# Performance work log

Hardware: AMD Instinct MI355X
Metric: run time of the kernel (lower is better)

The kernel has to match this reference:

```python
import jax, jax.numpy as jnp
import numpy as np
import math

B, S, D, H = 4, 512, 1024, 16
DH = D // H
DQ = D // 4
MIN_STEPS, MAX_STEPS = 4, 12
THR = 1e-4


def lin(t, w, b):
    # torch Linear convention: w is (out, in)
    return jnp.einsum('...i,oi->...o', t, w) + b


def gelu(t):
    return jax.nn.gelu(t, approximate=False)  # torch nn.GELU() exact


def layernorm(t, g, b):
    m = t.mean(-1, keepdims=True)
    v = jnp.mean(jnp.square(t - m), axis=-1, keepdims=True)
    return (t - m) * jax.lax.rsqrt(v + 1e-5) * g + b


def _forward(h, x, ig_w1, ig_b1, ig_w2, ig_b2, wq, bq, wk, bk, wv, bv, wo, bo,
             g1_w1, g1_b1, g1_w2, g1_b2, gate_logits, ln_g, ln_b,
             sp_w1, sp_b1, sp_w2, sp_b2):
    # adaptive step count: steps = base + floor(sigmoid(MLP(mean_pool(h))).mean() * extra)
    pooled = h.mean(axis=1)  # (B, D)
    extra = jax.nn.sigmoid(lin(gelu(lin(pooled, sp_w1, sp_b1)), sp_w2, sp_b2)).mean()
    num_steps = jnp.minimum(
        MIN_STEPS + jnp.floor(extra * (MAX_STEPS - MIN_STEPS)).astype(jnp.int32), MAX_STEPS)

    gw = jax.nn.softmax(gate_logits)  # gate weights over the 3 gates
    scale = 1.0 / math.sqrt(DH)

    def step(carry, i):
        h, active = carry
        # G1 gate (G2/G3 multiply zero memory/expert outputs -> drop)
        G1 = jax.nn.sigmoid(lin(gelu(lin(h, g1_w1, g1_b1)), g1_w2, g1_b2)) * gw[0]
        # Phi: input-gated blend + raw multi-head self-attention
        gate = jax.nn.sigmoid(
            lin(gelu(lin(jnp.concatenate([h, x], axis=-1), ig_w1, ig_b1)), ig_w2, ig_b2))
        blended = gate * h + (1.0 - gate) * x
        q = lin(blended, wq, bq).reshape(B, S, H, DH)
        k = lin(blended, wk, bk).reshape(B, S, H, DH)
        v = lin(blended, wv, bv).reshape(B, S, H, DH)
        attn = jax.nn.softmax(jnp.einsum('bqhd,bkhd->bhqk', q, k) * scale, axis=-1)
        ctx = jnp.einsum('bhqk,bkhd->bqhd', attn, v).reshape(B, S, D)
        phi = lin(ctx, wo, bo)
        h_new = layernorm(h + G1 * phi, ln_g, ln_b)
        res = jnp.linalg.norm(h_new - h) / (jnp.linalg.norm(h) + 1e-8)
        act_i = active & (i < num_steps)
        h = jnp.where(act_i, h_new, h)
        active = act_i & jnp.logical_not((i >= MIN_STEPS) & (res < THR))
        return (h, active), None

    (h, _), _ = jax.lax.scan(step, (h, jnp.array(True)), jnp.arange(MAX_STEPS))
    return h


def setup_inputs() -> dict:
    key = jax.random.key(0)
    ks = jax.random.split(key, 16)
    f32 = jnp.float32

    def W(k, out_d, in_d):
        return jax.random.normal(k, (out_d, in_d), f32) * (1.0 / np.sqrt(in_d))

    return {
        'h': jax.random.normal(ks[0], (B, S, D), f32),
        'x': jax.random.normal(ks[1], (B, S, D), f32),
        # PhiLayer input_gate: Linear(2D, D/4) -> GELU -> Linear(D/4, D) -> Sigmoid
        'ig_w1': W(ks[2], DQ, 2 * D), 'ig_b1': jnp.zeros((DQ,), f32),
        'ig_w2': W(ks[3], D, DQ), 'ig_b2': jnp.zeros((D,), f32),
        # QKV / out projections (xavier-ish, zero bias)
        'wq': W(ks[4], D, D), 'bq': jnp.zeros((D,), f32),
        'wk': W(ks[5], D, D), 'bk': jnp.zeros((D,), f32),
        'wv': W(ks[6], D, D), 'bv': jnp.zeros((D,), f32),
        'wo': W(ks[7], D, D), 'bo': jnp.zeros((D,), f32),
        # Gating gate #1 MLP (only G1 contributes; memory/experts are zero)
        'g1_w1': W(ks[8], DQ, D), 'g1_b1': jnp.zeros((DQ,), f32),
        'g1_w2': W(ks[9], D, DQ), 'g1_b2': jnp.zeros((D,), f32),
        'gate_logits': jnp.ones((3,), f32),  # nn.Parameter(torch.ones(3))
        # LayerNorm
        'ln_g': jnp.ones((D,), f32), 'ln_b': jnp.zeros((D,), f32),
        # step predictor: Linear(D, D/4) -> GELU -> Linear(D/4, 1)
        'sp_w1': W(ks[10], DQ, D), 'sp_b1': jnp.zeros((DQ,), f32),
        'sp_w2': W(ks[11], 1, DQ), 'sp_b2': jnp.zeros((1,), f32),
    }


def reference(h, x, ig_w1, ig_b1, ig_w2, ig_b2, wq, bq, wk, bk, wv, bv, wo, bo,
              g1_w1, g1_b1, g1_w2, g1_b2, gate_logits, ln_g, ln_b,
              sp_w1, sp_b1, sp_w2, sp_b2):
    return _forward(h, x, ig_w1, ig_b1, ig_w2, ig_b2, wq, bq, wk, bk, wv, bv, wo, bo,
                    g1_w1, g1_b1, g1_w2, g1_b2, gate_logits, ln_g, ln_b,
                    sp_w1, sp_b1, sp_w2, sp_b2)
```

## Files before the change

kernel.cpp:

```cpp
#include <hip/hip_runtime.h>
#include <hip/hip_bf16.h>


#define B_   4
#define S_   512
#define D_   1024
#define H_   16
#define DH_  64
#define MSEQ 2048
#define GRID_ 512

typedef short short8 __attribute__((ext_vector_type(8)));
typedef float floatx4 __attribute__((ext_vector_type(4)));

static constexpr size_t OFF_H    = 0;
static constexpr size_t OFF_X    = 2097152;
static constexpr size_t OFF_HXB  = 4194304;
static constexpr size_t OFF_T2B  = 6291456;
static constexpr size_t OFF_T1B  = 6553600;
static constexpr size_t OFF_G1B  = 6815744;
static constexpr size_t OFF_QKVB = 7864320;
static constexpr size_t OFF_U    = 7864320;
static constexpr size_t OFF_CTXB = 11010048;
static constexpr size_t OFF_WARE = 12058624;
static constexpr size_t OFF_BIAS = 14811136;
static constexpr size_t OFF_POOL = 14817792;
static constexpr size_t OFF_SPT  = 14821888;
static constexpr size_t OFF_PPART= 14822912;
static constexpr size_t OFF_SCAL = 14888448;
static constexpr size_t OFF_XIG  = 14888960;

static constexpr int W_WIG1 = 0;
static constexpr int W_WIG2 = 524288;
static constexpr int W_WG1  = 786432;
static constexpr int W_WG2  = 1048576;
static constexpr int W_QKV  = 1310720;
static constexpr int W_WO   = 4456448;
static constexpr int W_TOT  = 5505024;
static constexpr int B_TOT  = 6656;

__device__ __forceinline__ float bf2f(unsigned int u) {
  return __uint_as_float((u & 0xFFFFu) << 16);
}
__device__ __forceinline__ short f2bs(float f) {
  __hip_bfloat16 b = __float2bfloat16(f);
  return *reinterpret_cast<short*>(&b);
}
__device__ __forceinline__ unsigned int pk2(float lo, float hi) {
  return (unsigned int)(unsigned short)f2bs(lo) | ((unsigned int)(unsigned short)f2bs(hi) << 16);
}
__device__ __forceinline__ float ldf(const void* p, size_t i, int f32m) {
  return f32m ? ((const float*)p)[i] : bf2f(((const unsigned short*)p)[i]);
}
__device__ __forceinline__ int f32mode(const void* lng) {
  return (((const unsigned int*)lng)[0] == 0x3F800000u) ? 1 : 0;
}
__device__ __forceinline__ float gelu_f(float x) {
  return 0.5f * x * (1.0f + erff(x * 0.70710678118654752440f));
}
__device__ __forceinline__ float sig_f(float x) {
  return 1.0f / (1.0f + expf(-x));
}
__device__ __forceinline__ void gl_lds16(const short* gp, short* lp) {
  __builtin_amdgcn_global_load_lds(
      (const __attribute__((address_space(1))) unsigned int*)gp,
      (__attribute__((address_space(3))) unsigned int*)lp, 16, 0, 0);
}
__device__ __forceinline__ float wave_sum(float v) {
  #pragma unroll
  for (int off = 32; off > 0; off >>= 1) v += __shfl_xor(v, off);
  return v;
}

struct RepackPtrs {
  const void* w[8];
  const void* b[8];
};

__global__ __launch_bounds__(256) void repack_all_kernel(
    const void* __restrict__ lng, RepackPtrs ps,
    short* __restrict__ wdst, float* __restrict__ bdst) {
  const int f32m = f32mode(lng);
  int i = blockIdx.x * 256 + threadIdx.x;
  if (i < W_TOT) {
    const int off[9] = {0, 524288, 786432, 1048576, 1310720, 2359296, 3407872, 4456448, W_TOT};
    int seg = 0;
    #pragma unroll
    for (int s = 1; s < 8; s++) seg += (i >= off[s]) ? 1 : 0;
    wdst[i] = f2bs(ldf(ps.w[seg], i - off[seg], f32m));
  } else if (i < W_TOT + B_TOT) {
    int j = i - W_TOT;
    const int off[9] = {0, 256, 1280, 1536, 2560, 3584, 4608, 5632, B_TOT};
    int seg = 0;
    #pragma unroll
    for (int s = 1; s < 8; s++) seg += (j >= off[s]) ? 1 : 0;
    bdst[j] = ldf(ps.b[seg], j - off[seg], f32m);
  }
}

__global__ __launch_bounds__(256) void cvt_in_kernel(
    const void* __restrict__ lng, const void* __restrict__ hb,
    const void* __restrict__ xb, float* __restrict__ h, float* __restrict__ x,
    short* __restrict__ hxb, int n) {
  int f32m = f32mode(lng);
  int i = blockIdx.x * 256 + threadIdx.x;
  if (i < n) {
    float hv = ldf(hb, i, f32m);
    float xv = ldf(xb, i, f32m);
    h[i] = hv;
    x[i] = xv;
    int row = i >> 10, col = i & 1023;
    hxb[(size_t)row * 2048 + col] = f2bs(hv);
    hxb[(size_t)row * 2048 + 1024 + col] = f2bs(xv);
  }
}

__global__ __launch_bounds__(256) void pool_s1_kernel(
    const float* __restrict__ H, float* __restrict__ part) {
  int b = blockIdx.x, c = blockIdx.y, tid = threadIdx.x;
  const float* p = H + ((size_t)b * S_ + c * 32) * D_;
  #pragma unroll
  for (int rep = 0; rep < 4; rep++) {
    int d = rep * 256 + tid;
    float s = 0.f;
    for (int r = 0; r < 32; r++) s += p[(size_t)r * D_ + d];
    part[((size_t)b * 16 + c) * D_ + d] = s;
  }
}
__global__ __launch_bounds__(256) void pool_s2_kernel(
    const float* __restrict__ part, float* __restrict__ pooled) {
  int i = blockIdx.x * 256 + threadIdx.x;
  int b = i >> 10, d = i & 1023;
  float s = 0.f;
  #pragma unroll
  for (int c = 0; c < 16; c++) s += part[((size_t)b * 16 + c) * D_ + d];
  pooled[i] = s * (1.0f / (float)S_);
}

__device__ __forceinline__ float blk_sum256(float v, float* sm, int tid) {
  #pragma unroll
  for (int off = 32; off > 0; off >>= 1) v += __shfl_xor(v, off);
  __syncthreads();
  if ((tid & 63) == 0) sm[tid >> 6] = v;
  __syncthreads();
  return sm[0] + sm[1] + sm[2] + sm[3];
}

__global__ __launch_bounds__(256) void sp1_kernel(
    const void* __restrict__ lng, const float* __restrict__ pooled,
    const void* __restrict__ w1, const void* __restrict__ b1,
    float* __restrict__ spt) {
  __shared__ float sm[4];
  const int f32m = f32mode(lng);
  int j = blockIdx.x, tid = threadIdx.x;
  float s[4] = {0.f, 0.f, 0.f, 0.f};
  #pragma unroll
  for (int r = 0; r < 4; r++) {
    int k = tid * 4 + r;
    float w = ldf(w1, (size_t)j * D_ + k, f32m);
    s[0] += pooled[k] * w;
    s[1] += pooled[1024 + k] * w;
    s[2] += pooled[2048 + k] * w;
    s[3] += pooled[3072 + k] * w;
  }
  #pragma unroll
  for (int b = 0; b < 4; b++) {
    float t = blk_sum256(s[b], sm, tid);
    __syncthreads();
    if (tid == 0) spt[b * 256 + j] = gelu_f(t + ldf(b1, j, f32m));
  }
}

__global__ __launch_bounds__(256) void sp2_kernel(
    const void* __restrict__ lng, const float* __restrict__ spt,
    const void* __restrict__ w2, const void* __restrict__ b2,
    const void* __restrict__ glog,
    int* __restrict__ num_steps, int* __restrict__ active, int* __restrict__ cur,
    float* __restrict__ gw0, float* __restrict__ ssd, float* __restrict__ ssh,
    int* __restrict__ cnt) {
  __shared__ float z[4];
  const int f32m = f32mode(lng);
  int tid = threadIdx.x;
  if (tid < 12) cnt[tid] = 0;
  int wave = tid >> 6, lane = tid & 63;
  {
    int b = wave;
    float s = spt[b * 256 + lane]       * ldf(w2, lane, f32m) +
              spt[b * 256 + lane + 64]  * ldf(w2, lane + 64, f32m) +
              spt[b * 256 + lane + 128] * ldf(w2, lane + 128, f32m) +
              spt[b * 256 + lane + 192] * ldf(w2, lane + 192, f32m);
    #pragma unroll
    for (int off = 32; off > 0; off >>= 1) s += __shfl_xor(s, off);
    if (lane == 0) z[b] = sig_f(s + ldf(b2, 0, f32m));
  }
  __syncthreads();
  if (tid == 0) {
    float extra = 0.25f * (z[0] + z[1] + z[2] + z[3]);
    int ns = 4 + (int)floorf(extra * 8.0f);
    if (ns > 12) ns = 12;
    *num_steps = ns;
    *active = 1;
    *cur = 1;
    *ssd = 0.f; *ssh = 0.f;
    float g0 = ldf(glog, 0, f32m);
    float g1 = ldf(glog, 1, f32m);
    float g2 = ldf(glog, 2, f32m);
    float mx = fmaxf(g0, fmaxf(g1, g2));
    float e0 = expf(g0 - mx), e1 = expf(g1 - mx), e2 = expf(g2 - mx);
    *gw0 = e0 / (e0 + e1 + e2);
  }
}

enum { EPI_NONE = 0, EPI_GELU = 1, EPI_SIGSCALE = 2, EPI_BLEND = 3, EPI_RESADD = 4,
       EPI_GELU_ADD = 5, EPI_F32NB = 6 };

template <int EPI, int BM, int BN>
__device__ __forceinline__ void mgemm_core(
    short* As, short* Bs,
    const short* __restrict__ A, int lda,
    const short* __restrict__ W, int ldw, const float* __restrict__ bias,
    int K, int N,
    float* __restrict__ Cf, short* __restrict__ Cb,
    const float* __restrict__ aux1, const float* __restrict__ aux2f,
    const short* __restrict__ aux2b, const float* __restrict__ scale_ptr,
    int m0, int n0) {
  constexpr int FM = (BM / 2) / 16;
  constexpr int FN = (BN / 2) / 16;
  constexpr int CPA = (BM / 16) / 4;
  constexpr int CPB = (BN / 16) / 4;
  const int tid = threadIdx.x;
  const int lane = tid & 63, wv_ = tid >> 6;
  const int wm = (wv_ >> 1) * (BM / 2), wn = (wv_ & 1) * (BN / 2);
  const int srow = lane >> 2, scol = (lane & 3) * 8;
  const int frow = lane & 15, fk = (lane >> 4) * 8;

  floatx4 acc[FM][FN];
  #pragma unroll
  for (int i = 0; i < FM; i++)
    #pragma unroll
    for (int j = 0; j < FN; j++) acc[i][j] = (floatx4){0.f, 0.f, 0.f, 0.f};

  auto stage = [&](int buf, int k0) {
    short* Ad = As + buf * (BM * 64);
    short* Bd = Bs + buf * (BN * 64);
    #pragma unroll
    for (int c = 0; c < CPA; c++) {
      int q = wv_ * CPA + c;
      const short* gp = A + (size_t)(m0 + q * 16 + srow) * lda + k0 + scol;
      gl_lds16(gp, Ad + q * 512);
      gl_lds16(gp + 32, Ad + BM * 32 + q * 512);
    }
    #pragma unroll
    for (int c = 0; c < CPB; c++) {
      int q = wv_ * CPB + c;
      const short* gp = W + (size_t)(n0 + q * 16 + srow) * ldw + k0 + scol;
      gl_lds16(gp, Bd + q * 512);
      gl_lds16(gp + 32, Bd + BN * 32 + q * 512);
    }
  };

  stage(0, 0);
  __syncthreads();

  int cur = 0;
  for (int k0 = 0; k0 < K; k0 += 64) {
    if (k0 + 64 < K) stage(cur ^ 1, k0 + 64);
    const short* Ab = As + cur * (BM * 64);
    const short* Bb = Bs + cur * (BN * 64);
    #pragma unroll
    for (int hlf = 0; hlf < 2; hlf++) {
      const short* Ah = Ab + hlf * BM * 32;
      const short* Bh = Bb + hlf * BN * 32;
      short8 a[FM], b[FN];
      #pragma unroll
      for (int i = 0; i < FM; i++)
        a[i] = *reinterpret_cast<const short8*>(&Ah[(wm + i * 16 + frow) * 32 + fk]);
      #pragma unroll
      for (int j = 0; j < FN; j++)
        b[j] = *reinterpret_cast<const short8*>(&Bh[(wn + j * 16 + frow) * 32 + fk]);
      #pragma unroll
      for (int i = 0; i < FM; i++)
        #pragma unroll
        for (int j = 0; j < FN; j++)
          acc[i][j] = __builtin_amdgcn_mfma_f32_16x16x32_bf16(a[i], b[j], acc[i][j], 0, 0, 0);
    }
    __syncthreads();
    cur ^= 1;
  }

  float gwv = 0.f;
  if (EPI == EPI_SIGSCALE) gwv = *scale_ptr;
  const int rq = (lane >> 4) * 4;
  #pragma unroll
  for (int i = 0; i < FM; i++) {
    #pragma unroll
    for (int j = 0; j < FN; j++) {
      int n = n0 + wn + j * 16 + (lane & 15);
      float bv = (EPI == EPI_F32NB) ? 0.f : bias[n];
      #pragma unroll
      for (int r = 0; r < 4; r++) {
        int m = m0 + wm + i * 16 + rq + r;
        size_t off = (size_t)m * N + n;
        float v = acc[i][j][r] + bv;
        if (EPI == EPI_GELU) {
          Cb[off] = f2bs(gelu_f(v));
        } else if (EPI == EPI_GELU_ADD) {
          if (aux1) v += aux1[off];
          Cb[off] = f2bs(gelu_f(v));
        } else if (EPI == EPI_SIGSCALE) {
          Cb[off] = f2bs(sig_f(v) * gwv);
        } else if (EPI == EPI_BLEND) {
          float s = sig_f(v);
          Cb[off] = f2bs(s * aux1[off] + (1.f - s) * aux2f[off]);
        } else if (EPI == EPI_RESADD) {
          Cf[off] = aux1[off] + bf2f((unsigned short)aux2b[off]) * v;
        } else if (EPI == EPI_F32NB) {
          Cf[off] = v;
        } else {
          Cb[off] = f2bs(v);
        }
      }
    }
  }
}

template <int EPI, int BM, int BN>
__global__ __launch_bounds__(256) void mgemm(
    const int* __restrict__ flag, const short* __restrict__ A, int lda,
    const short* __restrict__ W, int ldw, const float* __restrict__ bias,
    int K, int N,
    float* __restrict__ Cf, short* __restrict__ Cb,
    const float* __restrict__ aux1, const float* __restrict__ aux2f,
    const short* __restrict__ aux2b, const float* __restrict__ scale_ptr) {
  if (flag && *flag == 0) return;
  __shared__ short As[2 * BM * 64];
  __shared__ short Bs[2 * BN * 64];
  mgemm_core<EPI, BM, BN>(As, Bs, A, lda, W, ldw, bias, K, N, Cf, Cb,
                          aux1, aux2f, aux2b, scale_ptr,
                          blockIdx.y * BM, blockIdx.x * BN);
}

__global__ __launch_bounds__(256) void gate1_kernel(
    const int* __restrict__ flag, const short* __restrict__ hxb,
    const short* __restrict__ warena, const float* __restrict__ biasA,
    short* __restrict__ t2b, short* __restrict__ t1b,
    const float* __restrict__ xig, int kz0) {
  if (*flag == 0) return;
  __shared__ short As[2 * 64 * 64];
  __shared__ short Bs[2 * 64 * 64];
  if (blockIdx.z == 0)
    mgemm_core<EPI_GELU_ADD, 64, 64>(As, Bs, hxb, 2048, warena + W_WIG1, 2048,
                                     biasA + 0, kz0, 256, nullptr, t2b, xig,
                                     nullptr, nullptr, nullptr,
                                     blockIdx.y * 64, blockIdx.x * 64);
  else
    mgemm_core<EPI_GELU, 64, 64>(As, Bs, hxb, 2048, warena + W_WG1, 1024,
                                 biasA + 1280, 1024, 256, nullptr, t1b, nullptr,
                                 nullptr, nullptr, nullptr,
                                 blockIdx.y * 64, blockIdx.x * 64);
}

__global__ __launch_bounds__(256) void gate2_kernel(
    const int* __restrict__ flag, const short* __restrict__ t2b,
    const short* __restrict__ t1b, const short* __restrict__ warena,
    const float* __restrict__ biasA, short* __restrict__ bldb,
    short* __restrict__ g1b, const float* __restrict__ h,
    const float* __restrict__ xf, const float* __restrict__ gw0) {
  if (*flag == 0) return;
  __shared__ short As[2 * 128 * 64];
  __shared__ short Bs[2 * 64 * 64];
  if (blockIdx.z == 0)
    mgemm_core<EPI_BLEND, 128, 64>(As, Bs, t2b, 256, warena + W_WIG2, 256,
                                   biasA + 256, 256, 1024, nullptr, bldb, h, xf,
                                   nullptr, nullptr, blockIdx.y * 128, blockIdx.x * 64);
  else
    mgemm_core<EPI_SIGSCALE, 128, 64>(As, Bs, t1b, 256, warena + W_WG2, 256,
                                      biasA + 1536, 256, 1024, nullptr, g1b,
                                      nullptr, nullptr, nullptr, gw0,
                                      blockIdx.y * 128, blockIdx.x * 64);
}

#define AP_ 72
__global__ __launch_bounds__(256) void attn_kernel(
    const int* __restrict__ flag, const short* __restrict__ qkv,
    short* __restrict__ ctxb) {
  if (*flag == 0) return;
  __shared__ short Ks[2][64 * AP_];
  __shared__ short Vt[2][64 * AP_];
  __shared__ short Ps[64 * AP_];
  const int tid = threadIdx.x;
  const int lane = tid & 63, wv = tid >> 6;
  const int ln15 = lane & 15, quad = lane >> 4;
  const int qt = blockIdx.x, hh = blockIdx.y, b = blockIdx.z;
  const int wm = wv * 16;
  const size_t rowbase = (size_t)b * S_;
  const int hcol = hh * DH_;
  const float scale = 0.125f;

  short8 qa[2];
  {
    const short* qp = qkv + (rowbase + qt * 64 + wm + ln15) * 3072 + hcol + quad * 8;
    qa[0] = *reinterpret_cast<const short8*>(qp);
    qa[1] = *reinterpret_cast<const short8*>(qp + 32);
  }
  const int skk = tid >> 2, scg = (tid & 3) * 16;

  float mrow[4] = {-1e30f, -1e30f, -1e30f, -1e30f};
  float lrow[4] = {0.f, 0.f, 0.f, 0.f};
  floatx4 accO[4];
  #pragma unroll
  for (int j = 0; j < 4; j++) accO[j] = (floatx4){0.f, 0.f, 0.f, 0.f};

  uint4 rk0, rk1;
  short8 rv0, rv1;
  auto load_regs = [&](int kt) {
    const short* gk = qkv + (rowbase + kt * 64 + skk) * 3072 + 1024 + hcol + scg;
    rk0 = *reinterpret_cast<const uint4*>(gk);
    rk1 = *reinterpret_cast<const uint4*>(gk + 8);
    rv0 = *reinterpret_cast<const short8*>(gk + 1024);
    rv1 = *reinterpret_cast<const short8*>(gk + 1032);
  };
  auto write_lds = [&](int buf) {
    *reinterpret_cast<uint4*>(&Ks[buf][skk * AP_ + scg]) = rk0;
    *reinterpret_cast<uint4*>(&Ks[buf][skk * AP_ + scg + 8]) = rk1;
    #pragma unroll
    for (int j = 0; j < 8; j++) Vt[buf][(scg + j) * AP_ + skk] = rv0[j];
    #pragma unroll
    for (int j = 0; j < 8; j++) Vt[buf][(scg + 8 + j) * AP_ + skk] = rv1[j];
  };

  load_regs(0);
  write_lds(0);
  __syncthreads();

  int cur = 0;
  for (int kt = 0; kt < 8; kt++) {
    if (kt < 7) load_regs(kt + 1);

    floatx4 sc[4];
    #pragma unroll
    for (int nf = 0; nf < 4; nf++) {
      short8 b0 = *reinterpret_cast<const short8*>(&Ks[cur][(nf * 16 + ln15) * AP_ + quad * 8]);
      short8 b1 = *reinterpret_cast<const short8*>(&Ks[cur][(nf * 16 + ln15) * AP_ + 32 + quad * 8]);
      floatx4 s = (floatx4){0.f, 0.f, 0.f, 0.f};
      s = __builtin_amdgcn_mfma_f32_16x16x32_bf16(qa[0], b0, s, 0, 0, 0);
      s = __builtin_amdgcn_mfma_f32_16x16x32_bf16(qa[1], b1, s, 0, 0, 0);
      sc[nf] = s;
    }

    float prob[4][4];
    #pragma unroll
    for (int r = 0; r < 4; r++) {
      float lm = fmaxf(fmaxf(sc[0][r], sc[1][r]), fmaxf(sc[2][r], sc[3][r])) * scale;
      lm = fmaxf(lm, __shfl_xor(lm, 1));
      lm = fmaxf(lm, __shfl_xor(lm, 2));
      lm = fmaxf(lm, __shfl_xor(lm, 4));
      lm = fmaxf(lm, __shfl_xor(lm, 8));
      float mn = fmaxf(mrow[r], lm);
      float alpha = expf(mrow[r] - mn);
      float ls = 0.f;
      #pragma unroll
      for (int nf = 0; nf < 4; nf++) {
        float p = expf(sc[nf][r] * scale - mn);
        prob[nf][r] = p;
        ls += p;
      }
      ls += __shfl_xor(ls, 1);
      ls += __shfl_xor(ls, 2);
      ls += __shfl_xor(ls, 4);
      ls += __shfl_xor(ls, 8);
      lrow[r] = lrow[r] * alpha + ls;
      mrow[r] = mn;
      #pragma unroll
      for (int df = 0; df < 4; df++) accO[df][r] *= alpha;
    }
    #pragma unroll
    for (int nf = 0; nf < 4; nf++)
      #pragma unroll
      for (int r = 0; r < 4; r++)
        Ps[(wm + quad * 4 + r) * AP_ + nf * 16 + ln15] = f2bs(prob[nf][r]);

    short8 pa0 = *reinterpret_cast<const short8*>(&Ps[(wm + ln15) * AP_ + quad * 8]);
    short8 pa1 = *reinterpret_cast<const short8*>(&Ps[(wm + ln15) * AP_ + 32 + quad * 8]);
    #pragma unroll
    for (int df = 0; df < 4; df++) {
      short8 bv0 = *reinterpret_cast<const short8*>(&Vt[cur][(df * 16 + ln15) * AP_ + quad * 8]);
      short8 bv1 = *reinterpret_cast<const short8*>(&Vt[cur][(df * 16 + ln15) * AP_ + 32 + quad * 8]);
      accO[df] = __builtin_amdgcn_mfma_f32_16x16x32_bf16(pa0, bv0, accO[df], 0, 0, 0);
      accO[df] = __builtin_amdgcn_mfma_f32_16x16x32_bf16(pa1, bv1, accO[df], 0, 0, 0);
    }

    if (kt < 7) write_lds(cur ^ 1);
    __syncthreads();
    cur ^= 1;
  }

  float inv[4];
  #pragma unroll
  for (int r = 0; r < 4; r++) inv[r] = 1.0f / lrow[r];
  #pragma unroll
  for (int df = 0; df < 4; df++) {
    #pragma unroll
    for (int r = 0; r < 4; r++) {
      size_t off = (rowbase + qt * 64 + wm + quad * 4 + r) * 1024 + hcol + df * 16 + ln15;
      ctxb[off] = f2bs(accO[df][r] * inv[r]);
    }
  }
}

__global__ __launch_bounds__(256) void ln_kernel(
    int step_i, const int* __restrict__ flagp,
    const float* __restrict__ U, float* __restrict__ H, short* __restrict__ hxb,
    const void* __restrict__ g, const void* __restrict__ be,
    void* __restrict__ Out,
    float* __restrict__ ssd, float* __restrict__ ssh,
    int* __restrict__ active, int* __restrict__ cur,
    const int* __restrict__ num_steps, int* __restrict__ cnt) {
  const int flag = *flagp;
  const int f32m = f32mode(g);
  __shared__ float sdd[4], sdh[4];
  const int tid = threadIdx.x;
  const int wv = tid >> 6, lane = tid & 63;
  if (flag) {
    const int row = blockIdx.x * 4 + wv;
    const float4* u4 = reinterpret_cast<const float4*>(U + (size_t)row * D_);
    float4* h4 = reinterpret_cast<float4*>(H + (size_t)row * D_);
    float4 uv[4], hv[4];
    #pragma unroll
    for (int j = 0; j < 4; j++) uv[j] = u4[lane + 64 * j];
    #pragma unroll
    for (int j = 0; j < 4; j++) hv[j] = h4[lane + 64 * j];
    float s = 0.f;
    #pragma unroll
    for (int j = 0; j < 4; j++) s += (uv[j].x + uv[j].y) + (uv[j].z + uv[j].w);
    s = wave_sum(s);
    float mean = s * (1.0f / (float)D_);
    float4 d[4];
    float vv = 0.f;
    #pragma unroll
    for (int j = 0; j < 4; j++) {
      d[j].x = uv[j].x - mean; d[j].y = uv[j].y - mean;
      d[j].z = uv[j].z - mean; d[j].w = uv[j].w - mean;
      vv += d[j].x * d[j].x + d[j].y * d[j].y + d[j].z * d[j].z + d[j].w * d[j].w;
    }
    vv = wave_sum(vv);
    float rstd = rsqrtf(vv * (1.0f / (float)D_) + 1e-5f);
    float lsd = 0.f, lsh = 0.f;
    #pragma unroll
    for (int j = 0; j < 4; j++) {
      int c = (lane + 64 * j) * 4;
      float hn0 = d[j].x * rstd * ldf(g, c + 0, f32m) + ldf(be, c + 0, f32m);
      float hn1 = d[j].y * rstd * ldf(g, c + 1, f32m) + ldf(be, c + 1, f32m);
      float hn2 = d[j].z * rstd * ldf(g, c + 2, f32m) + ldf(be, c + 2, f32m);
      float hn3 = d[j].w * rstd * ldf(g, c + 3, f32m) + ldf(be, c + 3, f32m);
      float e0 = hn0 - hv[j].x, e1 = hn1 - hv[j].y, e2 = hn2 - hv[j].z, e3 = hn3 - hv[j].w;
      lsd += e0 * e0 + e1 * e1 + e2 * e2 + e3 * e3;
      lsh += hv[j].x * hv[j].x + hv[j].y * hv[j].y + hv[j].z * hv[j].z + hv[j].w * hv[j].w;
      float4 hnv = make_float4(hn0, hn1, hn2, hn3);
      h4[lane + 64 * j] = hnv;
      uint2 pw;
      pw.x = pk2(hn0, hn1);
      pw.y = pk2(hn2, hn3);
      *reinterpret_cast<uint2*>(hxb + (size_t)row * 2048 + c) = pw;
      if (f32m) {
        reinterpret_cast<float4*>(Out)[(size_t)row * 256 + lane + 64 * j] = hnv;
      } else {
        *reinterpret_cast<uint2*>((short*)Out + (size_t)row * 1024 + c) = pw;
      }
    }
    lsd = wave_sum(lsd);
    lsh = wave_sum(lsh);
    if (lane == 0) { sdd[wv] = lsd; sdh[wv] = lsh; }
    __syncthreads();
    if (tid == 0) {
      atomicAdd(ssd, (sdd[0] + sdd[1]) + (sdd[2] + sdd[3]));
      atomicAdd(ssh, (sdh[0] + sdh[1]) + (sdh[2] + sdh[3]));
    }
  }
  if (tid == 0) {
    __threadfence();
    int old = atomicAdd(&cnt[step_i], 1);
    if (old == (int)gridDim.x - 1) {
      if (flag && step_i >= 4) {
        float nd = atomicAdd(ssd, 0.0f);
        float nh = atomicAdd(ssh, 0.0f);
        float res = sqrtf(nd) / (sqrtf(nh) + 1e-8f);
        if (res < 1e-4f) *active = 0;
      }
      *cur = ((*active) && (step_i + 1 < *num_steps)) ? 1 : 0;
      *ssd = 0.f; *ssh = 0.f;
    }
  }
}

extern "C" void kernel_launch(void* const* d_in, const int* in_sizes, int n_in,
                              void* d_out, int out_size, void* d_ws, size_t ws_size,
                              hipStream_t stream) {
  (void)in_sizes; (void)n_in; (void)out_size;
  const void* h_in  = d_in[0];
  const void* x_in  = d_in[1];
  const void* glog  = d_in[18];
  const void* ln_g  = d_in[19];
  const void* ln_b  = d_in[20];
  const void* sp_w1 = d_in[21];
  const void* sp_b1 = d_in[22];
  const void* sp_w2 = d_in[23];
  const void* sp_b2 = d_in[24];

  RepackPtrs rp;
  rp.w[0] = d_in[2];  rp.w[1] = d_in[4];  rp.w[2] = d_in[14]; rp.w[3] = d_in[16];
  rp.w[4] = d_in[6];  rp.w[5] = d_in[8];  rp.w[6] = d_in[10]; rp.w[7] = d_in[12];
  rp.b[0] = d_in[3];  rp.b[1] = d_in[5];  rp.b[2] = d_in[15]; rp.b[3] = d_in[17];
  rp.b[4] = d_in[7];  rp.b[5] = d_in[9];  rp.b[6] = d_in[11]; rp.b[7] = d_in[13];

  float* wsf = (float*)d_ws;
  float* h      = wsf + OFF_H;
  float* xf     = wsf + OFF_X;
  short* hxb    = (short*)(wsf + OFF_HXB);
  short* t2b    = (short*)(wsf + OFF_T2B);
  short* t1b    = (short*)(wsf + OFF_T1B);
  short* g1b    = (short*)(wsf + OFF_G1B);
  short* qkvb   = (short*)(wsf + OFF_QKVB);
  float* u      = wsf + OFF_U;
  short* ctxb   = (short*)(wsf + OFF_CTXB);
  short* bldb   = ctxb;
  short* warena = (short*)(wsf + OFF_WARE);
  float* biasA  = wsf + OFF_BIAS;
  float* pooled = wsf + OFF_POOL;
  float* spt    = wsf + OFF_SPT;
  float* ppart  = wsf + OFF_PPART;
  float* xigf   = wsf + OFF_XIG;
  float* ssd    = wsf + OFF_SCAL + 0;
  float* ssh    = wsf + OFF_SCAL + 1;
  float* gw0    = wsf + OFF_SCAL + 2;
  int* ip        = (int*)(wsf + OFF_SCAL + 8);
  int* num_steps = ip + 0;
  int* active    = ip + 1;
  int* cur       = ip + 2;
  int* cnt       = ip + 4;

  const int NTOT = B_ * S_ * D_;

  const int use_xig = (ws_size >= (OFF_XIG + 524288) * sizeof(float)) ? 1 : 0;
  const int kz0 = use_xig ? 1024 : 2048;

  repack_all_kernel<<<(W_TOT + B_TOT + 255) / 256, 256, 0, stream>>>(ln_g, rp, warena, biasA);
  cvt_in_kernel<<<NTOT / 256, 256, 0, stream>>>(ln_g, h_in, x_in, h, xf, hxb, NTOT);
  if (use_xig) {
    mgemm<EPI_F32NB, 64, 64><<<dim3(4, 32), 256, 0, stream>>>(
        nullptr, hxb + 1024, 2048, warena + W_WIG1 + 1024, 2048, nullptr,
        1024, 256, xigf, nullptr, nullptr, nullptr, nullptr, nullptr);
  }
  pool_s1_kernel<<<dim3(4, 16), 256, 0, stream>>>(h, ppart);
  pool_s2_kernel<<<16, 256, 0, stream>>>(ppart, pooled);
  sp1_kernel<<<256, 256, 0, stream>>>(ln_g, pooled, sp_w1, sp_b1, spt);
  sp2_kernel<<<1, 256, 0, stream>>>(ln_g, spt, sp_w2, sp_b2, glog,
                                    num_steps, active, cur, gw0, ssd, ssh, cnt);

  for (int i = 0; i < 12; i++) {
    gate1_kernel<<<dim3(4, 32, 2), 256, 0, stream>>>(
        cur, hxb, warena, biasA, t2b, t1b, use_xig ? xigf : nullptr, kz0);
    gate2_kernel<<<dim3(16, 16, 2), 256, 0, stream>>>(cur, t2b, t1b, warena, biasA,
                                                      bldb, g1b, h, xf, gw0);
    mgemm<EPI_NONE, 128, 64><<<dim3(48, 16), 256, 0, stream>>>(
        cur, bldb, 1024, warena + W_QKV, 1024, biasA + 2560, 1024, 3072,
        nullptr, qkvb, nullptr, nullptr, nullptr, nullptr);
    attn_kernel<<<dim3(8, 16, 4), 256, 0, stream>>>(cur, qkvb, ctxb);
    mgemm<EPI_RESADD, 64, 64><<<dim3(16, 32), 256, 0, stream>>>(
        cur, ctxb, 1024, warena + W_WO, 1024, biasA + 5632, 1024, 1024,
        u, nullptr, h, nullptr, g1b, nullptr);
    ln_kernel<<<512, 256, 0, stream>>>(i, cur, u, h, hxb, ln_g, ln_b, d_out,
                                       ssd, ssh, active, cur, num_steps, cnt);
  }
}
```

Baseline: 1.150 ms.

## Fuse LayerNorm of previous step into gate1 GEMM with per-step flags

```diff
diff --git a/kernel.cpp b/kernel.cpp
--- a/kernel.cpp
+++ b/kernel.cpp
@@ -177,11 +177,12 @@
     const void* __restrict__ glog,
     int* __restrict__ num_steps, int* __restrict__ active, int* __restrict__ cur,
     float* __restrict__ gw0, float* __restrict__ ssd, float* __restrict__ ssh,
-    int* __restrict__ cnt) {
+    int* __restrict__ cnt, int* __restrict__ flags) {
   __shared__ float z[4];
   const int f32m = f32mode(lng);
   int tid = threadIdx.x;
-  if (tid < 12) cnt[tid] = 0;
+  if (tid < 16) cnt[tid] = 0;
+  if (tid >= 32 && tid < 45) flags[tid - 32] = 0;
   int wave = tid >> 6, lane = tid & 63;
   {
     int b = wave;
@@ -201,6 +202,7 @@
     *num_steps = ns;
     *active = 1;
     *cur = 1;
+    flags[0] = 1;
     *ssd = 0.f; *ssh = 0.f;
     float g0 = ldf(glog, 0, f32m);
     float g1 = ldf(glog, 1, f32m);
@@ -338,6 +340,171 @@
   mgemm_core<EPI, BM, BN>(As, Bs, A, lda, W, ldw, bias, K, N, Cf, Cb,
                           aux1, aux2f, aux2b, scale_ptr,
                           blockIdx.y * BM, blockIdx.x * BN);
+}
+
+__global__ __launch_bounds__(256) void gate1ln_kernel(
+    int step_i, int* __restrict__ flags, const int* __restrict__ num_steps,
+    const float* __restrict__ U, float* __restrict__ Hp,
+    const short* __restrict__ warena, const float* __restrict__ biasA,
+    short* __restrict__ t2b, short* __restrict__ t1b,
+    const float* __restrict__ xig,
+    const void* __restrict__ g, const void* __restrict__ be,
+    void* __restrict__ Out,
+    float* __restrict__ ssd, float* __restrict__ ssh, int* __restrict__ cnt) {
+  const int fprev = (step_i == 0) ? 1 : flags[step_i - 1];
+  if (!fprev) return;
+  __shared__ short Asw[32 * 1024];
+  __shared__ short Bs[64 * 64];
+  __shared__ float sdd[4], sdh[4];
+  const int nz = blockIdx.x, mb = blockIdx.y;
+  const int m0 = mb * 32;
+  const int tid = threadIdx.x, lane = tid & 63, wv = tid >> 6;
+  const int f32m = f32mode(g);
+  const int ns = *num_steps;
+  const int desig = (nz == 0);
+
+  const short* W1 = warena + ((nz < 4) ? W_WIG1 : W_WG1);
+  const int ldw1 = (nz < 4) ? 2048 : 1024;
+  const int ncol0 = (nz & 3) * 64;
+  const int srow = lane >> 2, scol = (lane & 3) * 8;
+
+  auto stageB = [&](int k0) {
+    const short* gp = W1 + (size_t)(ncol0 + wv * 16 + srow) * ldw1 + k0 + scol;
+    gl_lds16(gp, Bs + wv * 512);
+    gl_lds16(gp + 32, Bs + 64 * 32 + wv * 512);
+  };
+
+  float lsd = 0.f, lsh = 0.f;
+  if (step_i == 0) {
+    for (int r8 = 0; r8 < 8; r8++) {
+      const int lr = wv * 8 + r8;
+      const float4* h4 = reinterpret_cast<const float4*>(Hp + (size_t)(m0 + lr) * D_);
+      #pragma unroll
+      for (int j = 0; j < 4; j++) {
+        float4 hv = h4[lane + 64 * j];
+        int c = (lane + 64 * j) * 4;
+        uint2 pw;
+        pw.x = pk2(hv.x, hv.y);
+        pw.y = pk2(hv.z, hv.w);
+        int addr = lr * 1024 + ((((c >> 3) ^ (lr & 7)) << 3) | (c & 7));
+        *reinterpret_cast<uint2*>(&Asw[addr]) = pw;
+      }
+    }
+  } else {
+    for (int r8 = 0; r8 < 8; r8++) {
+      const int lr = wv * 8 + r8;
+      const int row = m0 + lr;
+      const float4* u4 = reinterpret_cast<const float4*>(U + (size_t)row * D_);
+      float4* h4 = reinterpret_cast<float4*>(Hp + (size_t)row * D_);
+      float4 uv[4], hv[4];
+      #pragma unroll
+      for (int j = 0; j < 4; j++) uv[j] = u4[lane + 64 * j];
+      #pragma unroll
+      for (int j = 0; j < 4; j++) hv[j] = h4[lane + 64 * j];
+      float s = 0.f;
+      #pragma unroll
+      for (int j = 0; j < 4; j++) s += (uv[j].x + uv[j].y) + (uv[j].z + uv[j].w);
+      s = wave_sum(s);
+      float mean = s * (1.0f / (float)D_);
+      float4 d[4];
+      float vv = 0.f;
+      #pragma unroll
+      for (int j = 0; j < 4; j++) {
+        d[j].x = uv[j].x - mean; d[j].y = uv[j].y - mean;
+        d[j].z = uv[j].z - mean; d[j].w = uv[j].w - mean;
+        vv += d[j].x * d[j].x + d[j].y * d[j].y + d[j].z * d[j].z + d[j].w * d[j].w;
+      }
+      vv = wave_sum(vv);
+      float rstd = rsqrtf(vv * (1.0f / (float)D_) + 1e-5f);
+      #pragma unroll
+      for (int j = 0; j < 4; j++) {
+        int c = (lane + 64 * j) * 4;
+        float hn0 = d[j].x * rstd * ldf(g, c + 0, f32m) + ldf(be, c + 0, f32m);
+        float hn1 = d[j].y * rstd * ldf(g, c + 1, f32m) + ldf(be, c + 1, f32m);
+        float hn2 = d[j].z * rstd * ldf(g, c + 2, f32m) + ldf(be, c + 2, f32m);
+        float hn3 = d[j].w * rstd * ldf(g, c + 3, f32m) + ldf(be, c + 3, f32m);
+        float e0 = hn0 - hv[j].x, e1 = hn1 - hv[j].y, e2 = hn2 - hv[j].z, e3 = hn3 - hv[j].w;
+        lsd += e0 * e0 + e1 * e1 + e2 * e2 + e3 * e3;
+        lsh += hv[j].x * hv[j].x + hv[j].y * hv[j].y + hv[j].z * hv[j].z + hv[j].w * hv[j].w;
+        uint2 pw;
+        pw.x = pk2(hn0, hn1);
+        pw.y = pk2(hn2, hn3);
+        int addr = lr * 1024 + ((((c >> 3) ^ (lr & 7)) << 3) | (c & 7));
+        *reinterpret_cast<uint2*>(&Asw[addr]) = pw;
+        if (desig) {
+          h4[lane + 64 * j] = make_float4(hn0, hn1, hn2, hn3);
+          if (f32m) {
+            reinterpret_cast<float4*>(Out)[(size_t)row * 256 + lane + 64 * j] =
+                make_float4(hn0, hn1, hn2, hn3);
+          } else {
+            *reinterpret_cast<uint2*>((short*)Out + (size_t)row * 1024 + c) = pw;
+          }
+        }
+      }
+    }
+    if (desig) {
+      lsd = wave_sum(lsd);
+      lsh = wave_sum(lsh);
+      if (lane == 0) { sdd[wv] = lsd; sdh[wv] = lsh; }
+      __syncthreads();
+      if (tid == 0) {
+        atomicAdd(ssd, (sdd[0] + sdd[1]) + (sdd[2] + sdd[3]));
+        atomicAdd(ssh, (sdh[0] + sdh[1]) + (sdh[2] + sdh[3]));
+        __threadfence();
+        int old = atomicAdd(&cnt[step_i], 1);
+        if (old == 63) {
+          float nd = atomicAdd(ssd, 0.0f);
+          float nh = atomicAdd(ssh, 0.0f);
+          float res = sqrtf(nd) / (sqrtf(nh) + 1e-8f);
+          int conv = ((step_i - 1) >= 4) && (res < 1e-4f);
+          flags[step_i] = (step_i < ns && !conv) ? 1 : 0;
+          *ssd = 0.f; *ssh = 0.f;
+        }
+      }
+    }
+  }
+  if (step_i > 0 && step_i >= ns) { return; }
+  const int frow = lane & 15, quad = lane >> 4, fk = quad * 8;
+  const int wm = (wv >> 1) * 16, wn = (wv & 1) * 32;
+  floatx4 acc[2];
+  acc[0] = (floatx4){0.f, 0.f, 0.f, 0.f};
+  acc[1] = (floatx4){0.f, 0.f, 0.f, 0.f};
+  for (int k0 = 0; k0 < 1024; k0 += 64) {
+    __syncthreads();
+    stageB(k0);
+    __syncthreads();
+    #pragma unroll
+    for (int hlf = 0; hlf < 2; hlf++) {
+      int grp = ((k0 + hlf * 32 + fk) >> 3);
+      int row_l = wm + frow;
+      short8 a = *reinterpret_cast<const short8*>(
+          &Asw[row_l * 1024 + ((grp ^ (row_l & 7)) << 3)]);
+      const short* Bh = Bs + hlf * 64 * 32;
+      #pragma unroll
+      for (int j = 0; j < 2; j++) {
+        short8 b = *reinterpret_cast<const short8*>(&Bh[(wn + j * 16 + frow) * 32 + fk]);
+        acc[j] = __builtin_amdgcn_mfma_f32_16x16x32_bf16(a, b, acc[j], 0, 0, 0);
+      }
+    }
+  }
+  const int rq = quad * 4;
+  #pragma unroll
+  for (int j = 0; j < 2; j++) {
+    int n = ncol0 + wn + j * 16 + (lane & 15);
+    float bv = biasA[((nz < 4) ? 0 : 1280) + n];
+    #pragma unroll
+    for (int r = 0; r < 4; r++) {
+      int m = m0 + wm + rq + r;
+      size_t off = (size_t)m * 256 + n;
+      float v = acc[j][r] + bv;
+      if (nz < 4) {
+        v += xig[off];
+        t2b[off] = f2bs(gelu_f(v));
+      } else {
+        t1b[off] = f2bs(gelu_f(v));
+      }
+    }
+  }
 }
 
 __global__ __launch_bounds__(256) void gate1_kernel(
@@ -638,6 +805,7 @@
   int* active    = ip + 1;
   int* cur       = ip + 2;
   int* cnt       = ip + 4;
+  int* flags     = ip + 36;
 
   const int NTOT = B_ * S_ * D_;
 
@@ -655,21 +823,40 @@
   pool_s2_kernel<<<16, 256, 0, stream>>>(ppart, pooled);
   sp1_kernel<<<256, 256, 0, stream>>>(ln_g, pooled, sp_w1, sp_b1, spt);
   sp2_kernel<<<1, 256, 0, stream>>>(ln_g, spt, sp_w2, sp_b2, glog,
-                                    num_steps, active, cur, gw0, ssd, ssh, cnt);
-
-  for (int i = 0; i < 12; i++) {
-    gate1_kernel<<<dim3(4, 32, 2), 256, 0, stream>>>(
-        cur, hxb, warena, biasA, t2b, t1b, use_xig ? xigf : nullptr, kz0);
-    gate2_kernel<<<dim3(16, 16, 2), 256, 0, stream>>>(cur, t2b, t1b, warena, biasA,
-                                                      bldb, g1b, h, xf, gw0);
-    mgemm<EPI_NONE, 128, 64><<<dim3(48, 16), 256, 0, stream>>>(
-        cur, bldb, 1024, warena + W_QKV, 1024, biasA + 2560, 1024, 3072,
-        nullptr, qkvb, nullptr, nullptr, nullptr, nullptr);
-    attn_kernel<<<dim3(8, 16, 4), 256, 0, stream>>>(cur, qkvb, ctxb);
-    mgemm<EPI_RESADD, 64, 64><<<dim3(16, 32), 256, 0, stream>>>(
-        cur, ctxb, 1024, warena + W_WO, 1024, biasA + 5632, 1024, 1024,
-        u, nullptr, h, nullptr, g1b, nullptr);
-    ln_kernel<<<512, 256, 0, stream>>>(i, cur, u, h, hxb, ln_g, ln_b, d_out,
+                                    num_steps, active, cur, gw0, ssd, ssh, cnt, flags);
+
+  if (use_xig) {
+    for (int i = 0; i < 12; i++) {
+      gate1ln_kernel<<<dim3(8, 64), 256, 0, stream>>>(
+          i, flags, num_steps, u, h, warena, biasA, t2b, t1b, xigf,
+          ln_g, ln_b, d_out, ssd, ssh, cnt);
+      gate2_kernel<<<dim3(16, 16, 2), 256, 0, stream>>>(flags + i, t2b, t1b, warena,
+                                                        biasA, bldb, g1b, h, xf, gw0);
+      mgemm<EPI_NONE, 128, 64><<<dim3(48, 16), 256, 0, stream>>>(
+          flags + i, bldb, 1024, warena + W_QKV, 1024, biasA + 2560, 1024, 3072,
+          nullptr, qkvb, nullptr, nullptr, nullptr, nullptr);
+      attn_kernel<<<dim3(8, 16, 4), 256, 0, stream>>>(flags + i, qkvb, ctxb);
+      mgemm<EPI_RESADD, 64, 64><<<dim3(16, 32), 256, 0, stream>>>(
+          flags + i, ctxb, 1024, warena + W_WO, 1024, biasA + 5632, 1024, 1024,
+          u, nullptr, h, nullptr, g1b, nullptr);
+    }
+    ln_kernel<<<512, 256, 0, stream>>>(12, flags + 11, u, h, hxb, ln_g, ln_b, d_out,
                                        ssd, ssh, active, cur, num_steps, cnt);
-  }
-}
+  } else {
+    for (int i = 0; i < 12; i++) {
+      gate1_kernel<<<dim3(4, 32, 2), 256, 0, stream>>>(
+          cur, hxb, warena, biasA, t2b, t1b, nullptr, kz0);
+      gate2_kernel<<<dim3(16, 16, 2), 256, 0, stream>>>(cur, t2b, t1b, warena, biasA,
+                                                        bldb, g1b, h, xf, gw0);
+      mgemm<EPI_NONE, 128, 64><<<dim3(48, 16), 256, 0, stream>>>(
+          cur, bldb, 1024, warena + W_QKV, 1024, biasA + 2560, 1024, 3072,
+          nullptr, qkvb, nullptr, nullptr, nullptr, nullptr);
+      attn_kernel<<<dim3(8, 16, 4), 256, 0, stream>>>(cur, qkvb, ctxb);
+      mgemm<EPI_RESADD, 64, 64><<<dim3(16, 32), 256, 0, stream>>>(
+          cur, ctxb, 1024, warena + W_WO, 1024, biasA + 5632, 1024, 1024,
+          u, nullptr, h, nullptr, g1b, nullptr);
+      ln_kernel<<<512, 256, 0, stream>>>(i, cur, u, h, hxb, ln_g, ln_b, d_out,
+                                         ssd, ssh, active, cur, num_steps, cnt);
+    }
+  }
+}
```

Measured after the change: 1.398 ms. +21.5%, slower.
